# Performance work log

Measured on AMD Instinct MI355X. Metric: run time of the kernel, lower is better.

Reference implementation:

```python
import jax, jax.numpy as jnp
import numpy as np

EPS = 1e-5

def layer_norm(x, g, b):
    m = jnp.mean(x, axis=-1, keepdims=True)
    v = jnp.var(x, axis=-1, keepdims=True)
    return (x - m) / jnp.sqrt(v + EPS) * g + b


def setup_inputs() -> dict:
    key = jax.random.key(0)
    ks = jax.random.split(key, 12)
    B, L, D = 4, 4096, 512
    DF = 2 * D  # dim * dim_ff_scale
    inp = {
        "x": jax.random.normal(ks[0], (B, L, D), dtype=jnp.float32),
        "hidden_real": jax.random.normal(ks[1], (B, D), dtype=jnp.float32),
        "hidden_imag": jax.random.normal(ks[2], (B, D), dtype=jnp.float32),
        # SpiralConv complex params (real/imag parts), as torch.randn cfloat
        "phazor_re": jax.random.normal(ks[3], (D,), dtype=jnp.float32),
        "phazor_im": jax.random.normal(ks[4], (D,), dtype=jnp.float32),
        "pinit_re": jax.random.normal(ks[5], (D,), dtype=jnp.float32),
        "pinit_im": jax.random.normal(ks[6], (D,), dtype=jnp.float32),
        # shared LayerNorm params
        "ln_g": jnp.ones((D,), dtype=jnp.float32),
        "ln_b": jnp.zeros((D,), dtype=jnp.float32),
        # FFN params
        "w1": jax.random.normal(ks[7], (D, DF), dtype=jnp.float32) * (1.0 / np.sqrt(D)),
        "b1": jnp.zeros((DF,), dtype=jnp.float32),
        "w2": jax.random.normal(ks[8], (DF, D), dtype=jnp.float32) * (1.0 / np.sqrt(DF)),
        "b2": jnp.zeros((D,), dtype=jnp.float32),
    }
    return inp


def reference(x, hidden_real, hidden_imag, phazor_re, phazor_im,
              pinit_re, pinit_im, ln_g, ln_b, w1, b1, w2, b2):
    B, L, D = x.shape
    p = jax.lax.complex(phazor_re, phazor_im)
    pinit = jax.lax.complex(pinit_re, pinit_im)
    hidden_last = jax.lax.complex(hidden_real, hidden_imag)

    # phazor = p/|p| * exp(-|p|)  (unit direction, decaying magnitude)
    absp = jnp.abs(p)
    phazor = p / absp * jnp.exp(-absp)

    # phazor_progression[t, d] = phazor[d] ** t
    t = jnp.arange(L, dtype=jnp.float32)
    prog = jnp.exp(t[:, None] * jnp.log(phazor)[None, :])  # [L, D] complex
    filt = prog * pinit[None, :]                            # [L, D]

    x_res = x
    xn = layer_norm(x, ln_g, ln_b)

    # FFT long convolution along sequence, zero-padded to 2L (linear conv)
    filt_fft = jnp.fft.fft(filt, n=2 * L, axis=0)           # [2L, D]
    x_fft = jnp.fft.fft(xn, n=2 * L, axis=1)                # [B, 2L, D]
    conv = jnp.fft.ifft(filt_fft[None, :, :] * x_fft, axis=1)[:, :L, :]

    hidden = conv + hidden_last[:, None, :] * prog[None, :, :] * phazor[None, None, :]

    y = hidden.real + x_res
    yn = layer_norm(y, ln_g, ln_b)
    h = yn @ w1 + b1
    h = h * jax.nn.sigmoid(h)  # SiLU; dropout=0 (eval) is identity
    out = h @ w2 + b2 + y
    return out, hidden
```

## Files before the change

### kernel.cpp

```cpp
#include <hip/hip_runtime.h>
#include <hip/hip_bf16.h>
#include <math.h>

#define BB 4
#define LL 4096
#define DD 512
#define DF 1024
#define CHUNKS 64
#define LC 64
#define HALF_ROWS 8192

typedef __bf16 bf16x8 __attribute__((ext_vector_type(8)));
typedef float f32x4 __attribute__((ext_vector_type(4)));

__device__ inline void get_phazor(const float* __restrict__ pre, const float* __restrict__ pim,
                                  int d, float& ar, float& ai) {
    float pr = pre[d], pi = pim[d];
    float ab = sqrtf(pr * pr + pi * pi);
    float sc = expf(-ab) / ab;
    ar = pr * sc;
    ai = pi * sc;
}

__global__ __launch_bounds__(256) void k_wt(const float* __restrict__ w1, const float* __restrict__ w2,
                                            __bf16* __restrict__ w1t, __bf16* __restrict__ w2t) {
    __shared__ float tile[32][33];
    const float* src;
    __bf16* dst;
    int R, C;
    if (blockIdx.y == 0) { src = w1; dst = w1t; R = DD; C = DF; }
    else                 { src = w2; dst = w2t; R = DF; C = DD; }
    int ntx = C / 32;
    int c0 = (blockIdx.x % ntx) * 32, r0 = (blockIdx.x / ntx) * 32;
    int tx = threadIdx.x & 31, ty = threadIdx.x >> 5;
#pragma unroll
    for (int i = 0; i < 32; i += 8)
        tile[ty + i][tx] = src[(size_t)(r0 + ty + i) * C + c0 + tx];
    __syncthreads();
#pragma unroll
    for (int i = 0; i < 32; i += 8)
        dst[(size_t)(c0 + ty + i) * R + r0 + tx] = (__bf16)tile[tx][ty + i];
}

__global__ __launch_bounds__(256) void k_xstats(const float* __restrict__ x, float* __restrict__ xstats) {
    int wave = threadIdx.x >> 6, lane = threadIdx.x & 63;
    size_t row = (size_t)blockIdx.x * 4 + wave;
    const float4* xr = reinterpret_cast<const float4*>(x + row * DD) + lane * 2;
    float4 a = xr[0], b = xr[1];
    float s = a.x + a.y + a.z + a.w + b.x + b.y + b.z + b.w;
    float q = a.x * a.x + a.y * a.y + a.z * a.z + a.w * a.w +
              b.x * b.x + b.y * b.y + b.z * b.z + b.w * b.w;
#pragma unroll
    for (int off = 32; off; off >>= 1) {
        s += __shfl_down(s, off);
        q += __shfl_down(q, off);
    }
    if (lane == 0) {
        float m = s * (1.0f / DD);
        float v = q * (1.0f / DD) - m * m;
        xstats[row * 2 + 0] = m;
        xstats[row * 2 + 1] = rsqrtf(v + 1e-5f);
    }
}

__global__ __launch_bounds__(512) void k_scan_partial(
    const float* __restrict__ x, const float* __restrict__ xstats,
    const float* __restrict__ pre, const float* __restrict__ pim,
    const float* __restrict__ pinr, const float* __restrict__ pini,
    const float* __restrict__ g, const float* __restrict__ bvec,
    float* __restrict__ carry) {
    int d = threadIdx.x;
    int c = blockIdx.x % CHUNKS, b = blockIdx.x / CHUNKS;
    float ar, ai;
    get_phazor(pre, pim, d, ar, ai);
    float pr = pinr[d], pi = pini[d];
    float gd = g[d], bd = bvec[d];
    float hr = 0.f, hi = 0.f;
    int l0 = c * LC;
    const float* xp = x + ((size_t)b * LL + l0) * DD + d;
    const float* st = xstats + ((size_t)b * LL + l0) * 2;
    for (int i = 0; i < LC; i++) {
        float m = st[2 * i], r = st[2 * i + 1];
        float xn = (xp[(size_t)i * DD] - m) * r * gd + bd;
        float ur = pr * xn, ui = pi * xn;
        float t = ar * hr - ai * hi + ur;
        hi = ar * hi + ai * hr + ui;
        hr = t;
    }
    size_t idx = ((size_t)blockIdx.x * DD + d) * 2;
    carry[idx] = hr;
    carry[idx + 1] = hi;
}

__global__ __launch_bounds__(512) void k_chunk_scan(
    const float* __restrict__ hr0, const float* __restrict__ hi0,
    const float* __restrict__ pre, const float* __restrict__ pim,
    const float* __restrict__ carry, float* __restrict__ carry_in) {
    int d = threadIdx.x, b = blockIdx.x;
    float ar, ai;
    get_phazor(pre, pim, d, ar, ai);
    float sr = ar, si = ai;
#pragma unroll
    for (int i = 0; i < 6; i++) {
        float t = sr * sr - si * si;
        si = 2.f * sr * si;
        sr = t;
    }
    float cr = hr0[b * DD + d], ci = hi0[b * DD + d];
    for (int k = 0; k < CHUNKS; k++) {
        size_t idx = (((size_t)b * CHUNKS + k) * DD + d) * 2;
        carry_in[idx] = cr;
        carry_in[idx + 1] = ci;
        float tr = carry[idx], ti = carry[idx + 1];
        float t = sr * cr - si * ci + tr;
        ci = sr * ci + si * cr + ti;
        cr = t;
    }
}

template <int MODE>
__global__ __launch_bounds__(512) void k_scan_out(
    const float* __restrict__ x, const float* __restrict__ xstats,
    const float* __restrict__ pre, const float* __restrict__ pim,
    const float* __restrict__ pinr, const float* __restrict__ pini,
    const float* __restrict__ g, const float* __restrict__ bvec,
    const float* __restrict__ carry_in,
    float* __restrict__ out_y, float* __restrict__ hid) {
    int d = threadIdx.x;
    int c = blockIdx.x % CHUNKS, b = blockIdx.x / CHUNKS;
    float ar, ai;
    get_phazor(pre, pim, d, ar, ai);
    float pr = pinr[d], pi = pini[d];
    float gd = g[d], bd = bvec[d];
    size_t cidx = ((size_t)blockIdx.x * DD + d) * 2;
    float hr = carry_in[cidx], hi = carry_in[cidx + 1];
    int l0 = c * LC;
    const float* xp = x + ((size_t)b * LL + l0) * DD + d;
    const float* st = xstats + ((size_t)b * LL + l0) * 2;
    for (int i = 0; i < LC; i++) {
        float m = st[2 * i], r = st[2 * i + 1];
        float xv = xp[(size_t)i * DD];
        float xn = (xv - m) * r * gd + bd;
        float ur = pr * xn, ui = pi * xn;
        float t = ar * hr - ai * hi + ur;
        hi = ar * hi + ai * hr + ui;
        hr = t;
        size_t row = (size_t)b * LL + l0 + i;
        if constexpr (MODE == 0) {
            out_y[row * DD + d] = hr + xv;
        } else if constexpr (MODE == 1) {
            hid[row * DD + d] = hr;
        } else if constexpr (MODE == 2) {
            reinterpret_cast<float2*>(hid)[row * DD + d] = make_float2(hr, hi);
        } else {
            out_y[row * DD + d] = hr + xv;
            hid[row * DD + d] = hr;
        }
    }
}

__global__ __launch_bounds__(256) void k_ynorm(const float* __restrict__ y,
                                               const float* __restrict__ g, const float* __restrict__ bvec,
                                               __bf16* __restrict__ yn) {
    int wave = threadIdx.x >> 6, lane = threadIdx.x & 63;
    size_t row = (size_t)blockIdx.x * 4 + wave;
    const float4* yr = reinterpret_cast<const float4*>(y + row * DD) + lane * 2;
    float4 a = yr[0], b = yr[1];
    float s = a.x + a.y + a.z + a.w + b.x + b.y + b.z + b.w;
    float q = a.x * a.x + a.y * a.y + a.z * a.z + a.w * a.w +
              b.x * b.x + b.y * b.y + b.z * b.z + b.w * b.w;
#pragma unroll
    for (int off = 32; off; off >>= 1) {
        s += __shfl_xor(s, off);
        q += __shfl_xor(q, off);
    }
    float m = s * (1.0f / DD);
    float r = rsqrtf(q * (1.0f / DD) - m * m + 1e-5f);
    int dbase = lane * 8;
    const float4* gp = reinterpret_cast<const float4*>(g + dbase);
    const float4* bp = reinterpret_cast<const float4*>(bvec + dbase);
    float4 g0 = gp[0], g1 = gp[1], b0 = bp[0], b1 = bp[1];
    bf16x8 o;
    o[0] = (__bf16)((a.x - m) * r * g0.x + b0.x);
    o[1] = (__bf16)((a.y - m) * r * g0.y + b0.y);
    o[2] = (__bf16)((a.z - m) * r * g0.z + b0.z);
    o[3] = (__bf16)((a.w - m) * r * g0.w + b0.w);
    o[4] = (__bf16)((b.x - m) * r * g1.x + b1.x);
    o[5] = (__bf16)((b.y - m) * r * g1.y + b1.y);
    o[6] = (__bf16)((b.z - m) * r * g1.z + b1.z);
    o[7] = (__bf16)((b.w - m) * r * g1.w + b1.w);
    *reinterpret_cast<bf16x8*>(yn + row * DD + dbase) = o;
}

template <int BM, int BN, int KDIM, int NDIM, int EPI>
__global__ __launch_bounds__(512) void k_gemm(
    const __bf16* __restrict__ A, const __bf16* __restrict__ Bt,
    const float* __restrict__ bias, const float* __restrict__ yadd,
    float* __restrict__ outf, __bf16* __restrict__ outb) {
    __shared__ __align__(16) __bf16 As[2][BM * 64];
    __shared__ __align__(16) __bf16 Bs[2][BN * 64];
    constexpr int NT = NDIM / BN;
    constexpr int MR = BM / 32;
    constexpr int NR = BN / 64;
    constexpr int LPT = BM / 64 + BN / 64;
    int nwg = gridDim.x;
    int bid = blockIdx.x;
    int swz = (bid & 7) * (nwg >> 3) + (bid >> 3);
    int m0 = (swz / NT) * BM;
    int n0 = (swz % NT) * BN;
    int tid = threadIdx.x;
    int wid = tid >> 6, lane = tid & 63;

    f32x4 acc[MR][NR] = {};

    int wm = (wid >> 2) * (BM / 2), wn = (wid & 3) * (BN / 4);
    int fr = lane & 15;
    int qbase = lane >> 4;

    auto stage = [&](int buf, int k0) {
#pragma unroll
        for (int i = 0; i < BM / 64; i++) {
            int c = tid + i * 512;
            int row = c >> 3, kq = c & 7;
            int kqg = kq ^ (row & 7);
            const __bf16* ga = A + (size_t)(m0 + row) * KDIM + k0 + kqg * 8;
            __bf16* la = &As[buf][(size_t)(i * 512 + wid * 64) * 8];
            __builtin_amdgcn_global_load_lds((const __attribute__((address_space(1))) unsigned int*)ga,
                                             (__attribute__((address_space(3))) unsigned int*)la, 16, 0, 0);
        }
#pragma unroll
        for (int i = 0; i < BN / 64; i++) {
            int c = tid + i * 512;
            int row = c >> 3, kq = c & 7;
            int kqg = kq ^ (row & 7);
            const __bf16* gb = Bt + (size_t)(n0 + row) * KDIM + k0 + kqg * 8;
            __bf16* lb = &Bs[buf][(size_t)(i * 512 + wid * 64) * 8];
            __builtin_amdgcn_global_load_lds((const __attribute__((address_space(1))) unsigned int*)gb,
                                             (__attribute__((address_space(3))) unsigned int*)lb, 16, 0, 0);
        }
    };

    auto compute = [&](int buf) {
#pragma unroll
        for (int ks = 0; ks < 2; ks++) {
            int q = ks * 4 + qbase;
            bf16x8 af[MR], bfv[NR];
#pragma unroll
            for (int mi = 0; mi < MR; mi++) {
                int R = wm + mi * 16 + fr;
                af[mi] = *reinterpret_cast<const bf16x8*>(&As[buf][R * 64 + ((q ^ (R & 7)) << 3)]);
            }
#pragma unroll
            for (int ni = 0; ni < NR; ni++) {
                int R = wn + ni * 16 + fr;
                bfv[ni] = *reinterpret_cast<const bf16x8*>(&Bs[buf][R * 64 + ((q ^ (R & 7)) << 3)]);
            }
            __builtin_amdgcn_s_setprio(1);
#pragma unroll
            for (int mi = 0; mi < MR; mi++)
#pragma unroll
                for (int ni = 0; ni < NR; ni++)
                    acc[mi][ni] = __builtin_amdgcn_mfma_f32_16x16x32_bf16(af[mi], bfv[ni],
                                                                          acc[mi][ni], 0, 0, 0);
            __builtin_amdgcn_s_setprio(0);
        }
    };

    stage(0, 0);
    int cur = 0;
    for (int k0 = 64; k0 < KDIM; k0 += 64) {
        stage(cur ^ 1, k0);
        asm volatile("s_waitcnt vmcnt(%0)" ::"i"(LPT) : "memory");
        __builtin_amdgcn_s_barrier();
        compute(cur);
        __builtin_amdgcn_s_barrier();
        cur ^= 1;
    }
    asm volatile("s_waitcnt vmcnt(0)" ::: "memory");
    __builtin_amdgcn_s_barrier();
    compute(cur);

    int orow = (lane >> 4) * 4;
    int ocol = lane & 15;
#pragma unroll
    for (int mi = 0; mi < MR; mi++) {
#pragma unroll
        for (int ni = 0; ni < NR; ni++) {
            int gr = m0 + wm + mi * 16 + orow;
            int gc = n0 + wn + ni * 16 + ocol;
            float bv = bias[gc];
#pragma unroll
            for (int j = 0; j < 4; j++) {
                float v = acc[mi][ni][j] + bv;
                size_t idx = (size_t)(gr + j) * NDIM + gc;
                if constexpr (EPI == 1) {
                    float sv = v / (1.0f + __expf(-v));
                    outb[idx] = (__bf16)sv;
                } else {
                    outf[idx] = v + yadd[idx];
                }
            }
        }
    }
}

extern "C" void kernel_launch(void* const* d_in, const int* in_sizes, int n_in,
                              void* d_out, int out_size, void* d_ws, size_t ws_size,
                              hipStream_t stream) {
    const float* x = (const float*)d_in[0];
    const float* hr0 = (const float*)d_in[1];
    const float* hi0 = (const float*)d_in[2];
    const float* pre = (const float*)d_in[3];
    const float* pim = (const float*)d_in[4];
    const float* pinr = (const float*)d_in[5];
    const float* pini = (const float*)d_in[6];
    const float* lng = (const float*)d_in[7];
    const float* lnb = (const float*)d_in[8];
    const float* w1 = (const float*)d_in[9];
    const float* b1 = (const float*)d_in[10];
    const float* w2 = (const float*)d_in[11];
    const float* b2 = (const float*)d_in[12];

    const size_t n = (size_t)BB * LL * DD;
    float* outp = (float*)d_out;
    char* hidbase = (char*)d_out + n * 4;
    float* hidp = (float*)hidbase;
    bool interleaved = (out_size >= (int)(3 * n));

    char* ws = (char*)d_ws;
    float* xstats = (float*)ws;      ws += (size_t)BB * LL * 2 * 4;
    float* carry = (float*)ws;       ws += (size_t)BB * CHUNKS * DD * 8;
    float* carry_in = (float*)ws;    ws += (size_t)BB * CHUNKS * DD * 8;
    __bf16* w1t = (__bf16*)ws;       ws += (size_t)DD * DF * 2;
    __bf16* w2t = (__bf16*)ws;       ws += (size_t)DF * DD * 2;
    char* ws_big = ws;
    const size_t SMALL = (size_t)(128 + 1024 + 1024 + 1024 + 1024) * 1024;
    const size_t NEED_FULL = SMALL + ((size_t)48 << 20);
    const size_t NEED_HALF = SMALL + ((size_t)24 << 20);

    k_wt<<<dim3((DD / 32) * (DF / 32), 2), 256, 0, stream>>>(w1, w2, w1t, w2t);
    k_xstats<<<(BB * LL) / 4, 256, 0, stream>>>(x, xstats);
    k_scan_partial<<<BB * CHUNKS, 512, 0, stream>>>(x, xstats, pre, pim, pinr, pini, lng, lnb, carry);
    k_chunk_scan<<<BB, 512, 0, stream>>>(hr0, hi0, pre, pim, carry, carry_in);

    if (!interleaved && ws_size >= NEED_FULL) {
        __bf16* yn = (__bf16*)ws_big;
        __bf16* h1 = (__bf16*)(ws_big + ((size_t)16 << 20));
        k_scan_out<3><<<BB * CHUNKS, 512, 0, stream>>>(x, xstats, pre, pim, pinr, pini, lng, lnb,
                                                       carry_in, outp, hidp);
        k_ynorm<<<(BB * LL) / 4, 256, 0, stream>>>(outp, lng, lnb, yn);
        k_gemm<256, 256, DD, DF, 1><<<(BB * LL / 256) * (DF / 256), 512, 0, stream>>>(
            yn, w1t, b1, nullptr, nullptr, h1);
        k_gemm<128, 256, DF, DD, 2><<<(BB * LL / 128) * (DD / 256), 512, 0, stream>>>(
            h1, w2t, b2, outp, outp, nullptr);
    } else if (!interleaved && ws_size >= NEED_HALF) {
        __bf16* yn_h = (__bf16*)ws_big;
        __bf16* h1_h = (__bf16*)(ws_big + ((size_t)8 << 20));
        k_scan_out<3><<<BB * CHUNKS, 512, 0, stream>>>(x, xstats, pre, pim, pinr, pini, lng, lnb,
                                                       carry_in, outp, hidp);
        for (int h = 0; h < 2; h++) {
            float* yh = outp + (size_t)h * HALF_ROWS * DD;
            k_ynorm<<<HALF_ROWS / 4, 256, 0, stream>>>(yh, lng, lnb, yn_h);
            k_gemm<256, 256, DD, DF, 1><<<(HALF_ROWS / 256) * (DF / 256), 512, 0, stream>>>(
                yn_h, w1t, b1, nullptr, nullptr, h1_h);
            k_gemm<128, 256, DF, DD, 2><<<(HALF_ROWS / 128) * (DD / 256), 512, 0, stream>>>(
                h1_h, w2t, b2, yh, yh, nullptr);
        }
    } else {
        __bf16* yn_h = (__bf16*)hidbase;
        __bf16* h1_h = (__bf16*)(hidbase + ((size_t)8 << 20));
        k_scan_out<0><<<BB * CHUNKS, 512, 0, stream>>>(x, xstats, pre, pim, pinr, pini, lng, lnb,
                                                       carry_in, outp, nullptr);
        for (int h = 0; h < 2; h++) {
            float* yh = outp + (size_t)h * HALF_ROWS * DD;
            k_ynorm<<<HALF_ROWS / 4, 256, 0, stream>>>(yh, lng, lnb, yn_h);
            k_gemm<256, 256, DD, DF, 1><<<(HALF_ROWS / 256) * (DF / 256), 512, 0, stream>>>(
                yn_h, w1t, b1, nullptr, nullptr, h1_h);
            k_gemm<128, 256, DF, DD, 2><<<(HALF_ROWS / 128) * (DD / 256), 512, 0, stream>>>(
                h1_h, w2t, b2, yh, yh, nullptr);
        }
        if (interleaved) {
            k_scan_out<2><<<BB * CHUNKS, 512, 0, stream>>>(x, xstats, pre, pim, pinr, pini, lng, lnb,
                                                           carry_in, nullptr, hidp);
        } else {
            k_scan_out<1><<<BB * CHUNKS, 512, 0, stream>>>(x, xstats, pre, pim, pinr, pini, lng, lnb,
                                                           carry_in, nullptr, hidp);
        }
    }
}
```

Measured before the change: 113.5 us.

## Fuse y layernorm into scan output and use 1024-thread GEMM blocks

The scan-output kernel gains a mode that keeps each chunk's y values in registers, reduces the per-row mean and variance across waves through shared memory, and writes the bf16 normalized activations directly. This removes the separate k_ynorm pass and its re-read of y on the full-workspace path. Independently, the GEMM kernels move to 16 waves per block, giving each wave fewer M-fragments and each thread fewer staging loads. The risks are higher register pressure from the 64-element yreg array and the fully unrolled loop in the scan kernel, and lower occupancy or different latency hiding in the GEMM.

```diff
diff --git a/kernel.cpp b/kernel.cpp
--- a/kernel.cpp
+++ b/kernel.cpp
@@ -125,7 +125,7 @@
     const float* __restrict__ pinr, const float* __restrict__ pini,
     const float* __restrict__ g, const float* __restrict__ bvec,
     const float* __restrict__ carry_in,
-    float* __restrict__ out_y, float* __restrict__ hid) {
+    float* __restrict__ out_y, float* __restrict__ hid, __bf16* __restrict__ yn) {
     int d = threadIdx.x;
     int c = blockIdx.x % CHUNKS, b = blockIdx.x / CHUNKS;
     float ar, ai;
@@ -137,6 +137,13 @@
     int l0 = c * LC;
     const float* xp = x + ((size_t)b * LL + l0) * DD + d;
     const float* st = xstats + ((size_t)b * LL + l0) * 2;
+
+    float yreg[LC];
+    __shared__ float sm[LC][8][2];
+    __shared__ float2 stats[LC];
+    int w = d >> 6, lane = d & 63;
+
+#pragma unroll
     for (int i = 0; i < LC; i++) {
         float m = st[2 * i], r = st[2 * i + 1];
         float xv = xp[(size_t)i * DD];
@@ -152,9 +159,44 @@
             hid[row * DD + d] = hr;
         } else if constexpr (MODE == 2) {
             reinterpret_cast<float2*>(hid)[row * DD + d] = make_float2(hr, hi);
-        } else {
+        } else if constexpr (MODE == 3) {
             out_y[row * DD + d] = hr + xv;
             hid[row * DD + d] = hr;
+        } else {
+            float yv = hr + xv;
+            out_y[row * DD + d] = yv;
+            hid[row * DD + d] = hr;
+            yreg[i] = yv;
+            float s = yv, q = yv * yv;
+#pragma unroll
+            for (int off = 32; off; off >>= 1) {
+                s += __shfl_xor(s, off);
+                q += __shfl_xor(q, off);
+            }
+            if (lane == 0) { sm[i][w][0] = s; sm[i][w][1] = q; }
+        }
+    }
+
+    if constexpr (MODE == 4) {
+        __syncthreads();
+        {
+            int r = d >> 3, w2 = d & 7;
+            float s = sm[r][w2][0], q = sm[r][w2][1];
+            s += __shfl_down(s, 4); q += __shfl_down(q, 4);
+            s += __shfl_down(s, 2); q += __shfl_down(q, 2);
+            s += __shfl_down(s, 1); q += __shfl_down(q, 1);
+            if (w2 == 0) {
+                float m = s * (1.0f / DD);
+                float v = q * (1.0f / DD) - m * m;
+                stats[r] = make_float2(m, rsqrtf(v + 1e-5f));
+            }
+        }
+        __syncthreads();
+#pragma unroll
+        for (int i = 0; i < LC; i++) {
+            float2 s2 = stats[i];
+            size_t row = (size_t)b * LL + l0 + i;
+            yn[row * DD + d] = (__bf16)((yreg[i] - s2.x) * s2.y * gd + bd);
         }
     }
 }
@@ -193,16 +235,16 @@
 }
 
 template <int BM, int BN, int KDIM, int NDIM, int EPI>
-__global__ __launch_bounds__(512) void k_gemm(
+__global__ __launch_bounds__(1024) void k_gemm(
     const __bf16* __restrict__ A, const __bf16* __restrict__ Bt,
     const float* __restrict__ bias, const float* __restrict__ yadd,
     float* __restrict__ outf, __bf16* __restrict__ outb) {
     __shared__ __align__(16) __bf16 As[2][BM * 64];
     __shared__ __align__(16) __bf16 Bs[2][BN * 64];
     constexpr int NT = NDIM / BN;
-    constexpr int MR = BM / 32;
+    constexpr int MR = BM / 64;
     constexpr int NR = BN / 64;
-    constexpr int LPT = BM / 64 + BN / 64;
+    constexpr int LPT = BM / 128 + BN / 128;
     int nwg = gridDim.x;
     int bid = blockIdx.x;
     int swz = (bid & 7) * (nwg >> 3) + (bid >> 3);
@@ -213,28 +255,28 @@
 
     f32x4 acc[MR][NR] = {};
 
-    int wm = (wid >> 2) * (BM / 2), wn = (wid & 3) * (BN / 4);
+    int wm = (wid >> 2) * (BM / 4), wn = (wid & 3) * (BN / 4);
     int fr = lane & 15;
     int qbase = lane >> 4;
 
     auto stage = [&](int buf, int k0) {
 #pragma unroll
-        for (int i = 0; i < BM / 64; i++) {
-            int c = tid + i * 512;
+        for (int i = 0; i < BM / 128; i++) {
+            int c = tid + i * 1024;
             int row = c >> 3, kq = c & 7;
             int kqg = kq ^ (row & 7);
             const __bf16* ga = A + (size_t)(m0 + row) * KDIM + k0 + kqg * 8;
-            __bf16* la = &As[buf][(size_t)(i * 512 + wid * 64) * 8];
+            __bf16* la = &As[buf][(size_t)(i * 1024 + wid * 64) * 8];
             __builtin_amdgcn_global_load_lds((const __attribute__((address_space(1))) unsigned int*)ga,
                                              (__attribute__((address_space(3))) unsigned int*)la, 16, 0, 0);
         }
 #pragma unroll
-        for (int i = 0; i < BN / 64; i++) {
-            int c = tid + i * 512;
+        for (int i = 0; i < BN / 128; i++) {
+            int c = tid + i * 1024;
             int row = c >> 3, kq = c & 7;
             int kqg = kq ^ (row & 7);
             const __bf16* gb = Bt + (size_t)(n0 + row) * KDIM + k0 + kqg * 8;
-            __bf16* lb = &Bs[buf][(size_t)(i * 512 + wid * 64) * 8];
+            __bf16* lb = &Bs[buf][(size_t)(i * 1024 + wid * 64) * 8];
             __builtin_amdgcn_global_load_lds((const __attribute__((address_space(1))) unsigned int*)gb,
                                              (__attribute__((address_space(3))) unsigned int*)lb, 16, 0, 0);
         }
@@ -346,45 +388,44 @@
     if (!interleaved && ws_size >= NEED_FULL) {
         __bf16* yn = (__bf16*)ws_big;
         __bf16* h1 = (__bf16*)(ws_big + ((size_t)16 << 20));
-        k_scan_out<3><<<BB * CHUNKS, 512, 0, stream>>>(x, xstats, pre, pim, pinr, pini, lng, lnb,
-                                                       carry_in, outp, hidp);
-        k_ynorm<<<(BB * LL) / 4, 256, 0, stream>>>(outp, lng, lnb, yn);
-        k_gemm<256, 256, DD, DF, 1><<<(BB * LL / 256) * (DF / 256), 512, 0, stream>>>(
+        k_scan_out<4><<<BB * CHUNKS, 512, 0, stream>>>(x, xstats, pre, pim, pinr, pini, lng, lnb,
+                                                       carry_in, outp, hidp, yn);
+        k_gemm<256, 256, DD, DF, 1><<<(BB * LL / 256) * (DF / 256), 1024, 0, stream>>>(
             yn, w1t, b1, nullptr, nullptr, h1);
-        k_gemm<128, 256, DF, DD, 2><<<(BB * LL / 128) * (DD / 256), 512, 0, stream>>>(
+        k_gemm<128, 256, DF, DD, 2><<<(BB * LL / 128) * (DD / 256), 1024, 0, stream>>>(
             h1, w2t, b2, outp, outp, nullptr);
     } else if (!interleaved && ws_size >= NEED_HALF) {
         __bf16* yn_h = (__bf16*)ws_big;
         __bf16* h1_h = (__bf16*)(ws_big + ((size_t)8 << 20));
         k_scan_out<3><<<BB * CHUNKS, 512, 0, stream>>>(x, xstats, pre, pim, pinr, pini, lng, lnb,
-                                                       carry_in, outp, hidp);
+                                                       carry_in, outp, hidp, nullptr);
         for (int h = 0; h < 2; h++) {
             float* yh = outp + (size_t)h * HALF_ROWS * DD;
             k_ynorm<<<HALF_ROWS / 4, 256, 0, stream>>>(yh, lng, lnb, yn_h);
-            k_gemm<256, 256, DD, DF, 1><<<(HALF_ROWS / 256) * (DF / 256), 512, 0, stream>>>(
+            k_gemm<256, 256, DD, DF, 1><<<(HALF_ROWS / 256) * (DF / 256), 1024, 0, stream>>>(
                 yn_h, w1t, b1, nullptr, nullptr, h1_h);
-            k_gemm<128, 256, DF, DD, 2><<<(HALF_ROWS / 128) * (DD / 256), 512, 0, stream>>>(
+            k_gemm<128, 256, DF, DD, 2><<<(HALF_ROWS / 128) * (DD / 256), 1024, 0, stream>>>(
                 h1_h, w2t, b2, yh, yh, nullptr);
         }
     } else {
         __bf16* yn_h = (__bf16*)hidbase;
         __bf16* h1_h = (__bf16*)(hidbase + ((size_t)8 << 20));
         k_scan_out<0><<<BB * CHUNKS, 512, 0, stream>>>(x, xstats, pre, pim, pinr, pini, lng, lnb,
-                                                       carry_in, outp, nullptr);
+                                                       carry_in, outp, nullptr, nullptr);
         for (int h = 0; h < 2; h++) {
             float* yh = outp + (size_t)h * HALF_ROWS * DD;
             k_ynorm<<<HALF_ROWS / 4, 256, 0, stream>>>(yh, lng, lnb, yn_h);
-            k_gemm<256, 256, DD, DF, 1><<<(HALF_ROWS / 256) * (DF / 256), 512, 0, stream>>>(
+            k_gemm<256, 256, DD, DF, 1><<<(HALF_ROWS / 256) * (DF / 256), 1024, 0, stream>>>(
                 yn_h, w1t, b1, nullptr, nullptr, h1_h);
-            k_gemm<128, 256, DF, DD, 2><<<(HALF_ROWS / 128) * (DD / 256), 512, 0, stream>>>(
+            k_gemm<128, 256, DF, DD, 2><<<(HALF_ROWS / 128) * (DD / 256), 1024, 0, stream>>>(
                 h1_h, w2t, b2, yh, yh, nullptr);
         }
         if (interleaved) {
             k_scan_out<2><<<BB * CHUNKS, 512, 0, stream>>>(x, xstats, pre, pim, pinr, pini, lng, lnb,
-                                                           carry_in, nullptr, hidp);
+                                                           carry_in, nullptr, hidp, nullptr);
         } else {
             k_scan_out<1><<<BB * CHUNKS, 512, 0, stream>>>(x, xstats, pre, pim, pinr, pini, lng, lnb,
-                                                           carry_in, nullptr, hidp);
-        }
-    }
-}
+                                                           carry_in, nullptr, hidp, nullptr);
+        }
+    }
+}
```

Measured after the change: 122.5 us. 7.9% more time.
